# Kernel tuning notes

Measured on AMD Instinct MI355X. Metric: run time of the kernel, lower is better.

Reference implementation:

```python
import jax, jax.numpy as jnp
import numpy as np

B, T, D, H = 4, 2048, 128, 8
HS = D // H          # head_size = 16
E, K = 8, 2          # n_experts, top_experts
FF = 4 * D           # expert hidden = 512
EPS = 1e-5


def setup_inputs() -> dict:
    key = jax.random.key(0)
    ks = jax.random.split(key, 10)
    s = 0.02
    return {
        "x": jax.random.normal(ks[0], (B, T, D), jnp.float32),
        "ln1_g": jnp.ones((D,), jnp.float32),
        "ln1_b": jnp.zeros((D,), jnp.float32),
        "wq": jax.random.normal(ks[1], (H, D, HS), jnp.float32) * s,
        "wk": jax.random.normal(ks[2], (H, D, HS), jnp.float32) * s,
        "wv": jax.random.normal(ks[3], (H, D, HS), jnp.float32) * s,
        "w_proj": jax.random.normal(ks[4], (D, D), jnp.float32) * s,
        "b_proj": jnp.zeros((D,), jnp.float32),
        "ln2_g": jnp.ones((D,), jnp.float32),
        "ln2_b": jnp.zeros((D,), jnp.float32),
        "w_gate": jax.random.normal(ks[5], (D, E), jnp.float32) * s,
        "w1": jax.random.normal(ks[6], (E, D, FF), jnp.float32) * s,
        "b1": jnp.zeros((E, FF), jnp.float32),
        "w2": jax.random.normal(ks[7], (E, FF, D), jnp.float32) * s,
        "b2": jnp.zeros((E, D), jnp.float32),
    }


def _layernorm(x, g, b):
    m = jnp.mean(x, axis=-1, keepdims=True)
    v = jnp.mean(jnp.square(x - m), axis=-1, keepdims=True)
    return (x - m) * jax.lax.rsqrt(v + EPS) * g + b


def reference(x, ln1_g, ln1_b, wq, wk, wv, w_proj, b_proj,
              ln2_g, ln2_b, w_gate, w1, b1, w2, b2):
    Bx, Tx, Dx = x.shape
    # --- attention (pre-LN) ---
    xn = _layernorm(x, ln1_g, ln1_b)
    q = jnp.einsum('btd,hde->bhte', xn, wq)
    k = jnp.einsum('btd,hde->bhte', xn, wk)
    v = jnp.einsum('btd,hde->bhte', xn, wv)
    scale = 1.0 / jnp.sqrt(jnp.asarray(HS, x.dtype))
    scores = jnp.einsum('bhte,bhse->bhts', q, k) * scale  # [B,H,T,T]
    causal = jnp.tril(jnp.ones((Tx, Tx), bool))
    scores = jnp.where(causal, scores, jnp.finfo(x.dtype).min)
    p = jax.nn.softmax(scores, axis=-1)
    attn = jnp.einsum('bhts,bhse->bthe', p, v).reshape(Bx, Tx, Dx)
    x = x + attn @ w_proj + b_proj
    # --- MoE feed-forward (pre-LN) ---
    xn2 = _layernorm(x, ln2_g, ln2_b)
    xf = xn2.reshape(-1, Dx)                 # [N, D], N = B*T
    logits = xf @ w_gate                     # [N, E]
    probs = jax.nn.softmax(logits, axis=-1)
    topv, topi = jax.lax.top_k(probs, K)     # [N, K]
    gate_w = topv / jnp.sum(topv, axis=-1, keepdims=True)
    # expert FFN evaluated densely per expert (grouped-GEMM equivalent)
    h = jax.nn.gelu(jnp.einsum('nd,edh->neh', xf, w1) + b1, approximate=False)
    eo = jnp.einsum('neh,ehd->ned', h, w2) + b2           # [N, E, D]
    sel = jnp.take_along_axis(eo, topi[:, :, None], axis=1)  # [N, K, D]
    ff = jnp.sum(gate_w[:, :, None] * sel, axis=1).reshape(x.shape)
    # Switch-style load-balancing aux loss
    f_e = jnp.sum(jax.nn.one_hot(topi, E, dtype=x.dtype), axis=(0, 1)) / (xf.shape[0] * K)
    p_e = jnp.mean(probs, axis=0)
    aux = E * jnp.sum(f_e * p_e)
    return x + ff, aux
```

## Files before the change

### kernel.cpp

```cpp
#include <hip/hip_runtime.h>
#include <math.h>

#define Bsz 4
#define T 2048
#define D 128
#define H 8
#define HS 16
#define E 8
#define FF 512
#define N (Bsz*T)
#define NQ (Bsz*H*T)
#define EPS 1e-5f
#define SCALE2 0.36067376f
#define SPLITS 8

typedef _Float16 h4 __attribute__((ext_vector_type(4)));
typedef _Float16 h2 __attribute__((ext_vector_type(2)));
typedef float f4 __attribute__((ext_vector_type(4)));
#define MFMA16 __builtin_amdgcn_mfma_f32_16x16x16f16
#define EXP2(x) __builtin_amdgcn_exp2f(x)

__device__ __forceinline__ float wave_sum(float v) {
#pragma unroll
  for (int off = 32; off >= 1; off >>= 1) v += __shfl_xor(v, off);
  return v;
}

__global__ void pack_moe(const float* __restrict__ w1, const float* __restrict__ w2,
                         _Float16* __restrict__ w1pk, _Float16* __restrict__ w2pk) {
  int ft = blockIdx.x, kd = blockIdx.y;
  int e = blockIdx.z >> 1, m = blockIdx.z & 1;
  int l = threadIdx.x, lg = l >> 4, lr = l & 15;
  h4 v;
  if (m == 0) {
    const float* src = w1 + (size_t)e * D * FF;
#pragma unroll
    for (int i = 0; i < 4; ++i)
      v[i] = (_Float16)src[(size_t)(16 * kd + 4 * lg + i) * FF + 16 * ft + lr];
    ((h4*)w1pk)[(((size_t)e * 32 + ft) * 8 + kd) * 64 + l] = v;
  } else {
    const float* src = w2 + (size_t)e * FF * D;
#pragma unroll
    for (int i = 0; i < 4; ++i)
      v[i] = (_Float16)src[(size_t)(16 * ft + 4 * lg + i) * D + 16 * kd + lr];
    ((h4*)w2pk)[(((size_t)e * 32 + ft) * 8 + kd) * 64 + l] = v;
  }
}

__global__ void pack_attn(const float* __restrict__ wq, const float* __restrict__ wk,
                          const float* __restrict__ wv, const float* __restrict__ wp,
                          _Float16* __restrict__ wqh, _Float16* __restrict__ wql,
                          _Float16* __restrict__ wph, _Float16* __restrict__ wpl) {
  int ot = blockIdx.x, kd = blockIdx.y, m = blockIdx.z;
  int l = threadIdx.x, lg = l >> 4, lr = l & 15;
  h4 vh, vl;
  if (m < 3) {
    const float* W = (m == 0 ? wq : (m == 1 ? wk : wv));
    float sc = (m == 0) ? SCALE2 : 1.f;
#pragma unroll
    for (int i = 0; i < 4; ++i) {
      float w = W[((size_t)ot * D + 16 * kd + 4 * lg + i) * HS + lr] * sc;
      _Float16 h = (_Float16)w;
      vh[i] = h;
      vl[i] = (_Float16)(w - (float)h);
    }
    size_t idx = (((size_t)m * 8 + ot) * 8 + kd) * 64 + l;
    ((h4*)wqh)[idx] = vh;
    ((h4*)wql)[idx] = vl;
  } else {
#pragma unroll
    for (int i = 0; i < 4; ++i) {
      float w = wp[(size_t)(16 * kd + 4 * lg + i) * D + 16 * ot + lr];
      _Float16 h = (_Float16)w;
      vh[i] = h;
      vl[i] = (_Float16)(w - (float)h);
    }
    size_t idx = ((size_t)ot * 8 + kd) * 64 + l;
    ((h4*)wph)[idx] = vh;
    ((h4*)wpl)[idx] = vl;
  }
}

__global__ __launch_bounds__(512) void qkv_mfma(
    const float* __restrict__ x, const float* __restrict__ g, const float* __restrict__ bln,
    const _Float16* __restrict__ wh, const _Float16* __restrict__ wl,
    _Float16* __restrict__ qh, _Float16* __restrict__ kh, _Float16* __restrict__ vTh) {
  __shared__ _Float16 xsh[16][136];
  __shared__ _Float16 xsl[16][136];
  int n0 = blockIdx.x * 16;
  int b = n0 >> 11, t0 = n0 & (T - 1);
  int tid = threadIdx.x;
  {
    int i = tid >> 5, c = tid & 31;
    float4 v = *(const float4*)(x + (size_t)(n0 + i) * D + 4 * c);
    float s  = v.x + v.y + v.z + v.w;
    float s2 = v.x*v.x + v.y*v.y + v.z*v.z + v.w*v.w;
#pragma unroll
    for (int off = 16; off >= 1; off >>= 1) { s += __shfl_xor(s, off); s2 += __shfl_xor(s2, off); }
    float m = s * (1.f / D);
    float var = s2 * (1.f / D) - m * m;
    float r = rsqrtf(var + EPS);
    float4 gg = *(const float4*)(g + 4 * c);
    float4 bb = *(const float4*)(bln + 4 * c);
    float o0 = (v.x - m) * r * gg.x + bb.x;
    float o1 = (v.y - m) * r * gg.y + bb.y;
    float o2 = (v.z - m) * r * gg.z + bb.z;
    float o3 = (v.w - m) * r * gg.w + bb.w;
    _Float16 h0 = (_Float16)o0, h1 = (_Float16)o1, h2_ = (_Float16)o2, h3 = (_Float16)o3;
    *(h4*)&xsh[i][4 * c] = (h4){h0, h1, h2_, h3};
    *(h4*)&xsl[i][4 * c] = (h4){(_Float16)(o0 - (float)h0), (_Float16)(o1 - (float)h1),
                                (_Float16)(o2 - (float)h2_), (_Float16)(o3 - (float)h3)};
  }
  __syncthreads();
  int ot = tid >> 6;
  int l = tid & 63, lg = l >> 4, lr = l & 15;
  h4 xfh[8], xfl[8];
#pragma unroll
  for (int kd = 0; kd < 8; ++kd) {
    xfh[kd] = *(const h4*)&xsh[lr][16 * kd + 4 * lg];
    xfl[kd] = *(const h4*)&xsl[lr][16 * kd + 4 * lg];
  }
  const h4* wbh = (const h4*)wh + l;
  const h4* wbl = (const h4*)wl + l;
  f4 aq = {0.f,0.f,0.f,0.f}, ak = aq, av = aq;
#pragma unroll
  for (int kd = 0; kd < 8; ++kd) {
    h4 wqh_ = wbh[((0 * 8 + ot) * 8 + kd) * 64];
    h4 wkh_ = wbh[((1 * 8 + ot) * 8 + kd) * 64];
    h4 wvh_ = wbh[((2 * 8 + ot) * 8 + kd) * 64];
    h4 wql_ = wbl[((0 * 8 + ot) * 8 + kd) * 64];
    h4 wkl_ = wbl[((1 * 8 + ot) * 8 + kd) * 64];
    h4 wvl_ = wbl[((2 * 8 + ot) * 8 + kd) * 64];
    aq = MFMA16(wqh_, xfh[kd], aq, 0, 0, 0);
    ak = MFMA16(wkh_, xfh[kd], ak, 0, 0, 0);
    av = MFMA16(xfh[kd], wvh_, av, 0, 0, 0);
    aq = MFMA16(wql_, xfh[kd], aq, 0, 0, 0);
    ak = MFMA16(wkl_, xfh[kd], ak, 0, 0, 0);
    av = MFMA16(xfl[kd], wvh_, av, 0, 0, 0);
    aq = MFMA16(wqh_, xfl[kd], aq, 0, 0, 0);
    ak = MFMA16(wkh_, xfl[kd], ak, 0, 0, 0);
    av = MFMA16(xfh[kd], wvl_, av, 0, 0, 0);
  }
  h4 q4 = {(_Float16)aq.x, (_Float16)aq.y, (_Float16)aq.z, (_Float16)aq.w};
  h4 k4 = {(_Float16)ak.x, (_Float16)ak.y, (_Float16)ak.z, (_Float16)ak.w};
  size_t qoff = ((size_t)(b * H + ot) * T + t0 + lr) * 16 + 4 * lg;
  *(h4*)(qh + qoff) = q4;
  *(h4*)(kh + qoff) = k4;
  h4 v4 = {(_Float16)av.x, (_Float16)av.y, (_Float16)av.z, (_Float16)av.w};
  *(h4*)(vTh + ((size_t)(b * H + ot) * 16 + lr) * T + t0 + 4 * lg) = v4;
}

__global__ __launch_bounds__(256) void attn_mfma(
    const _Float16* __restrict__ q, const _Float16* __restrict__ k,
    const _Float16* __restrict__ vT, float* __restrict__ part) {
  int bh = blockIdx.y;
  int p = blockIdx.x * 4 + (threadIdx.x >> 6);
  int c = 1;
  while (p >= 2 * c * (c - 1) + 4 * c) ++c;
  int rem = p - 2 * c * (c - 1);
  int qt = (c - 1) * 4 + rem / c;
  int s = rem % c;
  int glo = 4 * s;
  int ghi = min(glo + 4, qt + 1);
  int l = threadIdx.x & 63;
  int lg = l >> 4, lr = l & 15;
  int q0 = qt * 64;
  const h4* qp = (const h4*)(q + ((size_t)bh * T + q0 + lr) * 16 + 4 * lg);
  h4 qf[4];
#pragma unroll
  for (int nt = 0; nt < 4; ++nt) qf[nt] = qp[nt * 64];
  f4 o0 = {0.f,0.f,0.f,0.f}, o1 = o0, o2 = o0, o3 = o0;
  float L0 = 0.f, L1 = 0.f, L2 = 0.f, L3 = 0.f;
  h4 kf[4], vf[4], kf2[4], vf2[4];
#define LOADKV(G, KK, VV) do { \
    int k0g = (G) * 64; \
    const h4* kp = (const h4*)(k + ((size_t)bh * T + k0g + lr) * 16 + 4 * lg); \
    _Pragma("unroll") for (int mt = 0; mt < 4; ++mt) KK[mt] = kp[mt * 64]; \
    const h4* vp = (const h4*)(vT + ((size_t)bh * 16 + lr) * T + k0g + 4 * lg); \
    _Pragma("unroll") for (int mt = 0; mt < 4; ++mt) VV[mt] = vp[mt * 4]; \
  } while (0)
  LOADKV(glo, kf, vf);
  for (int g = glo; g < ghi; ++g) {
    bool more = (g + 1 < ghi);
    if (more) LOADKV(g + 1, kf2, vf2);
    f4 z = {0.f,0.f,0.f,0.f};
    f4 sc[4][4];
#pragma unroll
    for (int mt = 0; mt < 4; ++mt)
#pragma unroll
      for (int nt = 0; nt < 4; ++nt)
        sc[mt][nt] = MFMA16(kf[mt], qf[nt], z, 0, 0, 0);
    if (g == qt) {
#pragma unroll
      for (int mt = 0; mt < 4; ++mt)
#pragma unroll
        for (int nt = 0; nt < 4; ++nt) {
          int kb = 16 * mt + 4 * lg, qb = 16 * nt + lr;
          if (kb + 0 > qb) sc[mt][nt].x = -1e30f;
          if (kb + 1 > qb) sc[mt][nt].y = -1e30f;
          if (kb + 2 > qb) sc[mt][nt].z = -1e30f;
          if (kb + 3 > qb) sc[mt][nt].w = -1e30f;
        }
    }
#define PROC(NT, L, O) do { \
    h4 pf[4]; \
    _Pragma("unroll") for (int mt = 0; mt < 4; ++mt) { \
      f4 a = sc[mt][NT]; h4 pv; float ex; \
      ex = EXP2(a.x); L += ex; pv.x = (_Float16)ex; \
      ex = EXP2(a.y); L += ex; pv.y = (_Float16)ex; \
      ex = EXP2(a.z); L += ex; pv.z = (_Float16)ex; \
      ex = EXP2(a.w); L += ex; pv.w = (_Float16)ex; \
      pf[mt] = pv; } \
    _Pragma("unroll") for (int mt = 0; mt < 4; ++mt) \
      O = MFMA16(vf[mt], pf[mt], O, 0, 0, 0); \
  } while (0)
    PROC(0, L0, o0);
    PROC(1, L1, o1);
    PROC(2, L2, o2);
    PROC(3, L3, o3);
#undef PROC
    if (more) {
#pragma unroll
      for (int mt = 0; mt < 4; ++mt) { kf[mt] = kf2[mt]; vf[mt] = vf2[mt]; }
    }
  }
#undef LOADKV
  L0 += __shfl_xor(L0, 16); L0 += __shfl_xor(L0, 32);
  L1 += __shfl_xor(L1, 16); L1 += __shfl_xor(L1, 32);
  L2 += __shfl_xor(L2, 16); L2 += __shfl_xor(L2, 32);
  L3 += __shfl_xor(L3, 16); L3 += __shfl_xor(L3, 32);
  float* pb = part + (size_t)s * 18 * NQ;
  int nbase = bh * T + q0 + lr;
#define WR(NT, L, O) do { int n = nbase + 16 * NT; \
    pb[(4 * lg + 0) * NQ + n] = O.x; pb[(4 * lg + 1) * NQ + n] = O.y; \
    pb[(4 * lg + 2) * NQ + n] = O.z; pb[(4 * lg + 3) * NQ + n] = O.w; \
    if (lg == 0) pb[16 * NQ + n] = L; \
  } while (0)
  WR(0, L0, o0);
  WR(1, L1, o1);
  WR(2, L2, o2);
  WR(3, L3, o3);
#undef WR
}

__global__ __launch_bounds__(512) void comb_proj(
    const float* __restrict__ part,
    const _Float16* __restrict__ wpph, const _Float16* __restrict__ wppl,
    const float* __restrict__ bp, const float* __restrict__ x,
    const float* __restrict__ ln2g, const float* __restrict__ ln2b,
    float* __restrict__ x1, float* __restrict__ xn2, _Float16* __restrict__ xh) {
  __shared__ float xP[16][132];
  int n0 = blockIdx.x * 16;
  int b = n0 >> 11, t0 = n0 & (T - 1);
  int tid = threadIdx.x;
  int ns = (t0 >> 8) + 1;
  {
    int i = tid & 15, h = (tid >> 4) & 7, r = tid >> 7;
    int n = (b * H + h) * T + t0 + i;
    float a0 = 0.f, a1 = 0.f, a2 = 0.f, a3 = 0.f, L = 0.f;
    for (int s = 0; s < ns; ++s) {
      const float* pb = part + (size_t)s * 18 * NQ;
      L  += pb[16 * NQ + n];
      a0 += pb[(4 * r + 0) * NQ + n];
      a1 += pb[(4 * r + 1) * NQ + n];
      a2 += pb[(4 * r + 2) * NQ + n];
      a3 += pb[(4 * r + 3) * NQ + n];
    }
    float inv = 1.f / L;
    float4 o = {a0 * inv, a1 * inv, a2 * inv, a3 * inv};
    *(float4*)&xP[i][h * 16 + 4 * r] = o;
  }
  __syncthreads();
  int ot = tid >> 6;
  int l = tid & 63, lg = l >> 4, lr = l & 15;
  h4 afh[8], afl[8];
#pragma unroll
  for (int kd = 0; kd < 8; ++kd) {
    float4 v = *(const float4*)&xP[lr][16 * kd + 4 * lg];
    _Float16 h0 = (_Float16)v.x, h1 = (_Float16)v.y, h2_ = (_Float16)v.z, h3 = (_Float16)v.w;
    afh[kd] = (h4){h0, h1, h2_, h3};
    afl[kd] = (h4){(_Float16)(v.x - (float)h0), (_Float16)(v.y - (float)h1),
                   (_Float16)(v.z - (float)h2_), (_Float16)(v.w - (float)h3)};
  }
  const h4* wbh = (const h4*)wpph + l;
  const h4* wbl = (const h4*)wppl + l;
  f4 acc = {0.f,0.f,0.f,0.f};
#pragma unroll
  for (int kd = 0; kd < 8; ++kd) {
    h4 wh_ = wbh[(ot * 8 + kd) * 64];
    h4 wl_ = wbl[(ot * 8 + kd) * 64];
    acc = MFMA16(wh_, afh[kd], acc, 0, 0, 0);
    acc = MFMA16(wl_, afh[kd], acc, 0, 0, 0);
    acc = MFMA16(wh_, afl[kd], acc, 0, 0, 0);
  }
  int o = 16 * ot + 4 * lg;
  float4 xr = *(const float4*)(x + (size_t)(n0 + lr) * D + o);
  float4 bb = *(const float4*)(bp + o);
  float4 ov = {acc.x + xr.x + bb.x, acc.y + xr.y + bb.y,
               acc.z + xr.z + bb.z, acc.w + xr.w + bb.w};
  *(float4*)(x1 + (size_t)(n0 + lr) * D + o) = ov;
  __syncthreads();
  *(float4*)&xP[lr][o] = ov;
  __syncthreads();
  {
    int i = tid >> 5, c = tid & 31;
    float4 v = *(const float4*)&xP[i][4 * c];
    float s  = v.x + v.y + v.z + v.w;
    float s2 = v.x*v.x + v.y*v.y + v.z*v.z + v.w*v.w;
#pragma unroll
    for (int off = 16; off >= 1; off >>= 1) { s += __shfl_xor(s, off); s2 += __shfl_xor(s2, off); }
    float m = s * (1.f / D);
    float var = s2 * (1.f / D) - m * m;
    float r = rsqrtf(var + EPS);
    float4 gg = *(const float4*)(ln2g + 4 * c);
    float4 bv = *(const float4*)(ln2b + 4 * c);
    float4 on = {(v.x - m) * r * gg.x + bv.x, (v.y - m) * r * gg.y + bv.y,
                 (v.z - m) * r * gg.z + bv.z, (v.w - m) * r * gg.w + bv.w};
    *(float4*)(xn2 + (size_t)(n0 + i) * D + 4 * c) = on;
    h4 oh = {(_Float16)on.x, (_Float16)on.y, (_Float16)on.z, (_Float16)on.w};
    *(h4*)(xh + (size_t)(n0 + i) * D + 4 * c) = oh;
  }
}

__global__ void gate_part(const float* __restrict__ xn2, const float* __restrict__ wg,
                          int* __restrict__ wcnt, float* __restrict__ wpsum,
                          int4* __restrict__ tokinfo, float2* __restrict__ gws) {
  int lane = threadIdx.x;
  int blk = blockIdx.x;
  int n = blk * 64 + lane;
  const float4* xr = (const float4*)(xn2 + (size_t)n * D);
  float lg[E];
#pragma unroll
  for (int e = 0; e < E; ++e) lg[e] = 0.f;
  for (int dq = 0; dq < 32; ++dq) {
    float4 xv = xr[dq];
    int d = dq * 4;
#pragma unroll
    for (int e = 0; e < E; ++e)
      lg[e] += xv.x * wg[d*E + e] + xv.y * wg[(d+1)*E + e]
             + xv.z * wg[(d+2)*E + e] + xv.w * wg[(d+3)*E + e];
  }
  float mx = lg[0];
#pragma unroll
  for (int e = 1; e < E; ++e) mx = fmaxf(mx, lg[e]);
  float p[E]; float s = 0.f;
#pragma unroll
  for (int e = 0; e < E; ++e) { p[e] = __expf(lg[e] - mx); s += p[e]; }
  float invs = 1.f / s;
#pragma unroll
  for (int e = 0; e < E; ++e) p[e] *= invs;
#pragma unroll
  for (int e = 0; e < E; ++e) {
    float ve = wave_sum(p[e]);
    if (lane == 0) wpsum[blk * E + e] = ve;
  }
  int i1 = 0; float p1 = p[0];
#pragma unroll
  for (int e = 1; e < E; ++e) if (p[e] > p1) { p1 = p[e]; i1 = e; }
  int i2 = (i1 == 0) ? 1 : 0; float p2 = p[i2];
#pragma unroll
  for (int e = 0; e < E; ++e) if (e != i1 && p[e] > p2) { p2 = p[e]; i2 = e; }
  float gden = 1.f / (p1 + p2);
  unsigned long long lt = (1ULL << lane) - 1ULL;
  int woff0 = 0, woff1 = 0;
  int c0[E], ctot[E];
#pragma unroll
  for (int e = 0; e < E; ++e) {
    unsigned long long m0 = __ballot(i1 == e);
    c0[e] = __popcll(m0);
    if (i1 == e) woff0 = __popcll(m0 & lt);
  }
#pragma unroll
  for (int e = 0; e < E; ++e) {
    unsigned long long m1 = __ballot(i2 == e);
    if (i2 == e) woff1 = c0[e] + __popcll(m1 & lt);
    ctot[e] = c0[e] + __popcll(m1);
  }
  if (lane == 0) {
#pragma unroll
    for (int e = 0; e < E; ++e) wcnt[blk * E + e] = ctot[e];
  }
  tokinfo[n] = make_int4(i1, woff0, i2, woff1);
  gws[n] = make_float2(p1 * gden, p2 * gden);
}

__global__ void gate_scan(const int* __restrict__ wcnt, const float* __restrict__ wpsum,
                          int* __restrict__ wbase, int* __restrict__ ecnt,
                          float* __restrict__ psum) {
  __shared__ int sc[128 * E];
  __shared__ float sp[128 * E];
  int tid = threadIdx.x;
  for (int i = tid; i < 128 * E; i += 64) { sc[i] = wcnt[i]; sp[i] = wpsum[i]; }
  __syncthreads();
  if (tid < E) {
    int run = 0;
    for (int b = 0; b < 128; ++b) { wbase[b * E + tid] = run; run += sc[b * E + tid]; }
    ecnt[tid] = run;
  } else if (tid >= 16 && tid < 16 + E) {
    int e = tid - 16;
    float sum = 0.f;
    for (int b = 0; b < 128; ++b) sum += sp[b * E + e];
    psum[e] = sum;
  }
}

__global__ void gate_scatter(const int4* __restrict__ tokinfo, const float2* __restrict__ gws,
                             const int* __restrict__ wbase,
                             int* __restrict__ ltok, int* __restrict__ sidx,
                             float* __restrict__ gwn) {
  int lane = threadIdx.x;
  int blk = blockIdx.x;
  int n = blk * 64 + lane;
  int4 ti = tokinfo[n];
  float2 g = gws[n];
  int pos0 = wbase[blk * E + ti.x] + ti.y;
  int pos1 = wbase[blk * E + ti.z] + ti.w;
  ltok[ti.x * N + pos0] = n;
  ltok[ti.z * N + pos1] = n;
  sidx[2 * n]     = ti.x * N + pos0;
  sidx[2 * n + 1] = ti.z * N + pos1;
  gwn[2 * n]     = g.x;
  gwn[2 * n + 1] = g.y;
}

__global__ __launch_bounds__(256) void moe_mfma(
    const _Float16* __restrict__ xh, const _Float16* __restrict__ w1pk,
    const float* __restrict__ b1, const _Float16* __restrict__ w2pk,
    const float* __restrict__ b2, const int* __restrict__ ecnt,
    const int* __restrict__ ltok, float* __restrict__ eo) {
  int e = blockIdx.y;
  int cnt = ecnt[e];
  int t0 = blockIdx.x * 16;
  if (t0 >= cnt) return;
  __shared__ int toks[16];
  __shared__ f4 red[3][8][64];
  int tid = threadIdx.x;
  if (tid < 16)
    toks[tid] = (t0 + tid < cnt) ? ltok[e * N + t0 + tid] : -1;
  __syncthreads();
  int fh = tid >> 6;
  int l = tid & 63;
  int lg = l >> 4, lr = l & 15;
  int tok = toks[lr];
  const h4* xp = (const h4*)(xh + (size_t)(tok < 0 ? 0 : tok) * D + 4 * lg);
  h4 xf[8];
#pragma unroll
  for (int kd = 0; kd < 8; ++kd) xf[kd] = xp[kd * 4];
  f4 oacc[8];
#pragma unroll
  for (int dt = 0; dt < 8; ++dt) oacc[dt] = (f4){0.f,0.f,0.f,0.f};
  const float* b1e = b1 + e * FF;
  const h4* w1b = (const h4*)w1pk + ((size_t)e * 32 + 8 * fh) * 8 * 64 + l;
  const h4* w2b = (const h4*)w2pk + ((size_t)e * 32 + 8 * fh) * 8 * 64 + l;
#pragma unroll 2
  for (int ftl = 0; ftl < 8; ++ftl) {
    f4 ha = {0.f,0.f,0.f,0.f};
#pragma unroll
    for (int kd = 0; kd < 8; ++kd)
      ha = MFMA16(w1b[(ftl * 8 + kd) * 64], xf[kd], ha, 0, 0, 0);
    int ft = 8 * fh + ftl;
    float4 bb = *(const float4*)&b1e[16 * ft + 4 * lg];
    h4 pf;
    {
      float z;
      z = ha.x + bb.x; pf.x = (_Float16)(0.5f * z * (1.f + erff(z * 0.70710678f)));
      z = ha.y + bb.y; pf.y = (_Float16)(0.5f * z * (1.f + erff(z * 0.70710678f)));
      z = ha.z + bb.z; pf.z = (_Float16)(0.5f * z * (1.f + erff(z * 0.70710678f)));
      z = ha.w + bb.w; pf.w = (_Float16)(0.5f * z * (1.f + erff(z * 0.70710678f)));
    }
#pragma unroll
    for (int dt = 0; dt < 8; ++dt)
      oacc[dt] = MFMA16(w2b[(ftl * 8 + dt) * 64], pf, oacc[dt], 0, 0, 0);
  }
  if (fh >= 1) {
#pragma unroll
    for (int dt = 0; dt < 8; ++dt) red[fh - 1][dt][l] = oacc[dt];
  }
  __syncthreads();
  if (fh == 0 && tok >= 0) {
    const float* b2e = b2 + e * D;
    float* eop = eo + ((size_t)(e * N + t0 + lr)) * 128;
#pragma unroll
    for (int dt = 0; dt < 8; ++dt) {
      f4 r0 = red[0][dt][l], r1 = red[1][dt][l], r2 = red[2][dt][l];
      float4 bb = *(const float4*)&b2e[16 * dt + 4 * lg];
      float4 o4 = {oacc[dt].x + r0.x + r1.x + r2.x + bb.x,
                   oacc[dt].y + r0.y + r1.y + r2.y + bb.y,
                   oacc[dt].z + r0.z + r1.z + r2.z + bb.z,
                   oacc[dt].w + r0.w + r1.w + r2.w + bb.w};
      *(float4*)(eop + 16 * dt + 4 * lg) = o4;
    }
  }
}

__global__ void finalize_kernel(const float* __restrict__ x1, const float* __restrict__ eo,
                                const int* __restrict__ sidx, const float* __restrict__ gwn,
                                const float* __restrict__ psum, const int* __restrict__ ecnt,
                                float* __restrict__ out) {
  int idx = blockIdx.x * 256 + threadIdx.x;
  int n = idx >> 5, d4 = idx & 31;
  int i0 = sidx[2*n], i1 = sidx[2*n+1];
  float g0 = gwn[2*n], g1 = gwn[2*n+1];
  float4 a = ((const float4*)x1)[idx];
  float4 u = ((const float4*)eo)[(size_t)i0 * 32 + d4];
  float4 w = ((const float4*)eo)[(size_t)i1 * 32 + d4];
  float4 o = {a.x + g0*u.x + g1*w.x, a.y + g0*u.y + g1*w.y,
              a.z + g0*u.z + g1*w.z, a.w + g0*u.w + g1*w.w};
  ((float4*)out)[idx] = o;
  if (idx == 0) {
    float aux = 0.f;
    for (int e = 0; e < E; ++e)
      aux += ((float)ecnt[e] * (1.f / 16384.f)) * (psum[e] * (1.f / 8192.f));
    out[N * D] = 8.f * aux;
  }
}

extern "C" void kernel_launch(void* const* d_in, const int* in_sizes, int n_in,
                              void* d_out, int out_size, void* d_ws, size_t ws_size,
                              hipStream_t stream) {
  const float* x    = (const float*)d_in[0];
  const float* ln1g = (const float*)d_in[1];
  const float* ln1b = (const float*)d_in[2];
  const float* wq   = (const float*)d_in[3];
  const float* wk   = (const float*)d_in[4];
  const float* wv   = (const float*)d_in[5];
  const float* wp   = (const float*)d_in[6];
  const float* bp   = (const float*)d_in[7];
  const float* ln2g = (const float*)d_in[8];
  const float* ln2b = (const float*)d_in[9];
  const float* wg   = (const float*)d_in[10];
  const float* w1   = (const float*)d_in[11];
  const float* b1   = (const float*)d_in[12];
  const float* w2   = (const float*)d_in[13];
  const float* b2   = (const float*)d_in[14];
  float* out = (float*)d_out;
  float* ws = (float*)d_ws;
  const size_t M = 1u << 20;
  float* Bq = ws + 1 * M;
  _Float16* qh  = (_Float16*)(ws + 2 * M);
  _Float16* xh  = (_Float16*)(ws + 2 * M);
  _Float16* kh  = (_Float16*)(ws + 2 * M + M / 2);
  _Float16* vTh = (_Float16*)(ws + 3 * M);
  float* part = ws + 3 * M + M / 2;
  float* eo   = part;
  float* xn2  = ws + 13 * M + M / 2;
  _Float16* w1pk = (_Float16*)(ws + 14 * M + M / 2);
  _Float16* w2pk = (_Float16*)(ws + 14 * M + 3 * (M / 4));
  size_t G0 = 15 * M;
  int*    ltok   = (int*)(ws + G0);
  int*    sidx   = (int*)(ws + G0 + 65536);
  float*  gwn    = ws + G0 + 81920;
  float*  psum   = ws + G0 + 98304;
  int*    ecnt   = (int*)(ws + G0 + 98312);
  int*    wcnt   = (int*)(ws + G0 + 98320);
  float*  wpsum  = ws + G0 + 99344;
  int*    wbase  = (int*)(ws + G0 + 100368);
  int4*   tokinfo= (int4*)(ws + G0 + 101392);
  float2* gws    = (float2*)(ws + G0 + 134160);
  _Float16* wqkvh = (_Float16*)(ws + G0 + 150544);
  _Float16* wqkvl = (_Float16*)(ws + G0 + 175120);
  _Float16* wpph  = (_Float16*)(ws + G0 + 199696);
  _Float16* wppl  = (_Float16*)(ws + G0 + 207888);

  pack_moe<<<dim3(32, 8, 2 * E), 64, 0, stream>>>(w1, w2, w1pk, w2pk);
  pack_attn<<<dim3(8, 8, 4), 64, 0, stream>>>(wq, wk, wv, wp, wqkvh, wqkvl, wpph, wppl);
  qkv_mfma<<<N / 16, 512, 0, stream>>>(x, ln1g, ln1b, wqkvh, wqkvl, qh, kh, vTh);
  attn_mfma<<<dim3(36, Bsz * H), 256, 0, stream>>>(qh, kh, vTh, part);
  comb_proj<<<N / 16, 512, 0, stream>>>(part, wpph, wppl, bp, x, ln2g, ln2b, Bq, xn2, xh);
  gate_part<<<N / 64, 64, 0, stream>>>(xn2, wg, wcnt, wpsum, tokinfo, gws);
  gate_scan<<<1, 64, 0, stream>>>(wcnt, wpsum, wbase, ecnt, psum);
  gate_scatter<<<N / 64, 64, 0, stream>>>(tokinfo, gws, wbase, ltok, sidx, gwn);
  moe_mfma<<<dim3(N / 16, E), 256, 0, stream>>>(xh, w1pk, b1, w2pk, b2, ecnt, ltok, eo);
  finalize_kernel<<<(N * D / 4) / 256, 256, 0, stream>>>(Bq, eo, sidx, gwn, psum, ecnt, out);
}
```

Baseline: 112.3 us.

## Fuse gating into comb_proj and merge scan with scatter kernel

Gate logits, softmax, top-2 selection and per-block counting now run inside comb_proj on the LN2 output held in shared memory, so the fp32 xn2 buffer is neither written nor re-read. The single-block scan and the scatter kernel are merged into one kernel in which every block redundantly reloads all 512 per-block counts and computes the prefix sums itself. This cuts the launch count by two and removes a serial single-block step. The cost is that only 16 threads do the gating work in comb_proj, and each scatter block repeats the scan.

After: 115.7 us. +3.0%, slower.

```diff
diff --git a/kernel.cpp b/kernel.cpp
--- a/kernel.cpp
+++ b/kernel.cpp
@@ -19,12 +19,6 @@
 typedef float f4 __attribute__((ext_vector_type(4)));
 #define MFMA16 __builtin_amdgcn_mfma_f32_16x16x16f16
 #define EXP2(x) __builtin_amdgcn_exp2f(x)
-
-__device__ __forceinline__ float wave_sum(float v) {
-#pragma unroll
-  for (int off = 32; off >= 1; off >>= 1) v += __shfl_xor(v, off);
-  return v;
-}
 
 __global__ void pack_moe(const float* __restrict__ w1, const float* __restrict__ w2,
                          _Float16* __restrict__ w1pk, _Float16* __restrict__ w2pk) {
@@ -248,10 +242,14 @@
     const _Float16* __restrict__ wpph, const _Float16* __restrict__ wppl,
     const float* __restrict__ bp, const float* __restrict__ x,
     const float* __restrict__ ln2g, const float* __restrict__ ln2b,
-    float* __restrict__ x1, float* __restrict__ xn2, _Float16* __restrict__ xh) {
+    const float* __restrict__ wg,
+    float* __restrict__ x1, _Float16* __restrict__ xh,
+    int* __restrict__ wcnt, float* __restrict__ wpsum,
+    int4* __restrict__ tokinfo, float2* __restrict__ gws) {
   __shared__ float xP[16][132];
   int n0 = blockIdx.x * 16;
   int b = n0 >> 11, t0 = n0 & (T - 1);
+  int blk = blockIdx.x;
   int tid = threadIdx.x;
   int ns = (t0 >> 8) + 1;
   {
@@ -316,105 +314,113 @@
     float4 bv = *(const float4*)(ln2b + 4 * c);
     float4 on = {(v.x - m) * r * gg.x + bv.x, (v.y - m) * r * gg.y + bv.y,
                  (v.z - m) * r * gg.z + bv.z, (v.w - m) * r * gg.w + bv.w};
-    *(float4*)(xn2 + (size_t)(n0 + i) * D + 4 * c) = on;
     h4 oh = {(_Float16)on.x, (_Float16)on.y, (_Float16)on.z, (_Float16)on.w};
     *(h4*)(xh + (size_t)(n0 + i) * D + 4 * c) = oh;
-  }
-}
-
-__global__ void gate_part(const float* __restrict__ xn2, const float* __restrict__ wg,
-                          int* __restrict__ wcnt, float* __restrict__ wpsum,
-                          int4* __restrict__ tokinfo, float2* __restrict__ gws) {
-  int lane = threadIdx.x;
-  int blk = blockIdx.x;
-  int n = blk * 64 + lane;
-  const float4* xr = (const float4*)(xn2 + (size_t)n * D);
-  float lg[E];
-#pragma unroll
-  for (int e = 0; e < E; ++e) lg[e] = 0.f;
-  for (int dq = 0; dq < 32; ++dq) {
-    float4 xv = xr[dq];
-    int d = dq * 4;
-#pragma unroll
-    for (int e = 0; e < E; ++e)
-      lg[e] += xv.x * wg[d*E + e] + xv.y * wg[(d+1)*E + e]
-             + xv.z * wg[(d+2)*E + e] + xv.w * wg[(d+3)*E + e];
-  }
-  float mx = lg[0];
-#pragma unroll
-  for (int e = 1; e < E; ++e) mx = fmaxf(mx, lg[e]);
-  float p[E]; float s = 0.f;
-#pragma unroll
-  for (int e = 0; e < E; ++e) { p[e] = __expf(lg[e] - mx); s += p[e]; }
-  float invs = 1.f / s;
-#pragma unroll
-  for (int e = 0; e < E; ++e) p[e] *= invs;
-#pragma unroll
-  for (int e = 0; e < E; ++e) {
-    float ve = wave_sum(p[e]);
-    if (lane == 0) wpsum[blk * E + e] = ve;
-  }
-  int i1 = 0; float p1 = p[0];
-#pragma unroll
-  for (int e = 1; e < E; ++e) if (p[e] > p1) { p1 = p[e]; i1 = e; }
-  int i2 = (i1 == 0) ? 1 : 0; float p2 = p[i2];
-#pragma unroll
-  for (int e = 0; e < E; ++e) if (e != i1 && p[e] > p2) { p2 = p[e]; i2 = e; }
-  float gden = 1.f / (p1 + p2);
-  unsigned long long lt = (1ULL << lane) - 1ULL;
-  int woff0 = 0, woff1 = 0;
-  int c0[E], ctot[E];
-#pragma unroll
-  for (int e = 0; e < E; ++e) {
-    unsigned long long m0 = __ballot(i1 == e);
-    c0[e] = __popcll(m0);
-    if (i1 == e) woff0 = __popcll(m0 & lt);
-  }
-#pragma unroll
-  for (int e = 0; e < E; ++e) {
-    unsigned long long m1 = __ballot(i2 == e);
-    if (i2 == e) woff1 = c0[e] + __popcll(m1 & lt);
-    ctot[e] = c0[e] + __popcll(m1);
-  }
-  if (lane == 0) {
-#pragma unroll
-    for (int e = 0; e < E; ++e) wcnt[blk * E + e] = ctot[e];
-  }
-  tokinfo[n] = make_int4(i1, woff0, i2, woff1);
-  gws[n] = make_float2(p1 * gden, p2 * gden);
-}
-
-__global__ void gate_scan(const int* __restrict__ wcnt, const float* __restrict__ wpsum,
-                          int* __restrict__ wbase, int* __restrict__ ecnt,
-                          float* __restrict__ psum) {
-  __shared__ int sc[128 * E];
-  __shared__ float sp[128 * E];
-  int tid = threadIdx.x;
-  for (int i = tid; i < 128 * E; i += 64) { sc[i] = wcnt[i]; sp[i] = wpsum[i]; }
-  __syncthreads();
-  if (tid < E) {
+    *(float4*)&xP[i][4 * c] = on;
+  }
+  __syncthreads();
+  if (tid < 16) {
+    int n = n0 + tid;
+    float lgt[E];
+#pragma unroll
+    for (int e = 0; e < E; ++e) lgt[e] = 0.f;
+    for (int dq = 0; dq < 32; ++dq) {
+      float4 xv = *(const float4*)&xP[tid][4 * dq];
+      int d = dq * 4;
+#pragma unroll
+      for (int e = 0; e < E; ++e)
+        lgt[e] += xv.x * wg[d*E + e] + xv.y * wg[(d+1)*E + e]
+                + xv.z * wg[(d+2)*E + e] + xv.w * wg[(d+3)*E + e];
+    }
+    float mx = lgt[0];
+#pragma unroll
+    for (int e = 1; e < E; ++e) mx = fmaxf(mx, lgt[e]);
+    float p[E]; float s = 0.f;
+#pragma unroll
+    for (int e = 0; e < E; ++e) { p[e] = __expf(lgt[e] - mx); s += p[e]; }
+    float invs = 1.f / s;
+#pragma unroll
+    for (int e = 0; e < E; ++e) p[e] *= invs;
+#pragma unroll
+    for (int e = 0; e < E; ++e) {
+      float ve = p[e];
+      ve += __shfl_xor(ve, 8); ve += __shfl_xor(ve, 4);
+      ve += __shfl_xor(ve, 2); ve += __shfl_xor(ve, 1);
+      if (tid == 0) wpsum[blk * E + e] = ve;
+    }
+    int i1 = 0; float p1 = p[0];
+#pragma unroll
+    for (int e = 1; e < E; ++e) if (p[e] > p1) { p1 = p[e]; i1 = e; }
+    int i2 = (i1 == 0) ? 1 : 0; float p2 = p[i2];
+#pragma unroll
+    for (int e = 0; e < E; ++e) if (e != i1 && p[e] > p2) { p2 = p[e]; i2 = e; }
+    float gden = 1.f / (p1 + p2);
+    unsigned long long lt = (1ULL << tid) - 1ULL;
+    int woff0 = 0, woff1 = 0;
+    int c0[E], ctot[E];
+#pragma unroll
+    for (int e = 0; e < E; ++e) {
+      unsigned long long m0 = __ballot(i1 == e);
+      c0[e] = __popcll(m0);
+      if (i1 == e) woff0 = __popcll(m0 & lt);
+    }
+#pragma unroll
+    for (int e = 0; e < E; ++e) {
+      unsigned long long m1 = __ballot(i2 == e);
+      if (i2 == e) woff1 = c0[e] + __popcll(m1 & lt);
+      ctot[e] = c0[e] + __popcll(m1);
+    }
+    if (tid == 0) {
+#pragma unroll
+      for (int e = 0; e < E; ++e) wcnt[blk * E + e] = ctot[e];
+    }
+    tokinfo[n] = make_int4(i1, woff0, i2, woff1);
+    gws[n] = make_float2(p1 * gden, p2 * gden);
+  }
+}
+
+__global__ __launch_bounds__(64) void gate_scat(
+    const int* __restrict__ wcnt, const float* __restrict__ wpsum,
+    const int4* __restrict__ tokinfo, const float2* __restrict__ gws,
+    int* __restrict__ ltok, int* __restrict__ sidx, float* __restrict__ gwn,
+    int* __restrict__ ecnt, float* __restrict__ psum) {
+  __shared__ int pre[512 * E];
+  __shared__ int segsum[8][E];
+  int tid = threadIdx.x, blk = blockIdx.x;
+  for (int i = tid; i < 512 * E; i += 64) pre[i] = wcnt[i];
+  __syncthreads();
+  {
+    int e = tid & 7, seg = tid >> 3;
+    int s = 0;
+    for (int b = seg * 64; b < seg * 64 + 64; ++b) s += pre[b * E + e];
+    segsum[seg][e] = s;
+  }
+  __syncthreads();
+  if (tid < 8) {
     int run = 0;
-    for (int b = 0; b < 128; ++b) { wbase[b * E + tid] = run; run += sc[b * E + tid]; }
-    ecnt[tid] = run;
-  } else if (tid >= 16 && tid < 16 + E) {
+    for (int g = 0; g < 8; ++g) { int c = segsum[g][tid]; segsum[g][tid] = run; run += c; }
+    if (blk == 0) ecnt[tid] = run;
+  } else if (blk == 0 && tid >= 16 && tid < 24) {
     int e = tid - 16;
-    float sum = 0.f;
-    for (int b = 0; b < 128; ++b) sum += sp[b * E + e];
-    psum[e] = sum;
-  }
-}
-
-__global__ void gate_scatter(const int4* __restrict__ tokinfo, const float2* __restrict__ gws,
-                             const int* __restrict__ wbase,
-                             int* __restrict__ ltok, int* __restrict__ sidx,
-                             float* __restrict__ gwn) {
-  int lane = threadIdx.x;
-  int blk = blockIdx.x;
-  int n = blk * 64 + lane;
+    float s = 0.f;
+    for (int b = 0; b < 512; ++b) s += wpsum[b * E + e];
+    psum[e] = s;
+  }
+  __syncthreads();
+  {
+    int e = tid & 7, seg = tid >> 3;
+    int run = segsum[seg][e];
+    for (int b = seg * 64; b < seg * 64 + 64; ++b) {
+      int c = pre[b * E + e]; pre[b * E + e] = run; run += c;
+    }
+  }
+  __syncthreads();
+  int n = blk * 64 + tid;
   int4 ti = tokinfo[n];
   float2 g = gws[n];
-  int pos0 = wbase[blk * E + ti.x] + ti.y;
-  int pos1 = wbase[blk * E + ti.z] + ti.w;
+  int sb = n >> 4;
+  int pos0 = pre[sb * E + ti.x] + ti.y;
+  int pos1 = pre[sb * E + ti.z] + ti.w;
   ltok[ti.x * N + pos0] = n;
   ltok[ti.z * N + pos1] = n;
   sidx[2 * n]     = ti.x * N + pos0;
@@ -543,7 +549,6 @@
   _Float16* vTh = (_Float16*)(ws + 3 * M);
   float* part = ws + 3 * M + M / 2;
   float* eo   = part;
-  float* xn2  = ws + 13 * M + M / 2;
   _Float16* w1pk = (_Float16*)(ws + 14 * M + M / 2);
   _Float16* w2pk = (_Float16*)(ws + 14 * M + 3 * (M / 4));
   size_t G0 = 15 * M;
@@ -553,23 +558,21 @@
   float*  psum   = ws + G0 + 98304;
   int*    ecnt   = (int*)(ws + G0 + 98312);
   int*    wcnt   = (int*)(ws + G0 + 98320);
-  float*  wpsum  = ws + G0 + 99344;
-  int*    wbase  = (int*)(ws + G0 + 100368);
-  int4*   tokinfo= (int4*)(ws + G0 + 101392);
-  float2* gws    = (float2*)(ws + G0 + 134160);
-  _Float16* wqkvh = (_Float16*)(ws + G0 + 150544);
-  _Float16* wqkvl = (_Float16*)(ws + G0 + 175120);
-  _Float16* wpph  = (_Float16*)(ws + G0 + 199696);
-  _Float16* wppl  = (_Float16*)(ws + G0 + 207888);
+  float*  wpsum  = ws + G0 + 102416;
+  int4*   tokinfo= (int4*)(ws + G0 + 106512);
+  float2* gws    = (float2*)(ws + G0 + 139280);
+  _Float16* wqkvh = (_Float16*)(ws + G0 + 155664);
+  _Float16* wqkvl = (_Float16*)(ws + G0 + 180240);
+  _Float16* wpph  = (_Float16*)(ws + G0 + 204816);
+  _Float16* wppl  = (_Float16*)(ws + G0 + 213008);
 
   pack_moe<<<dim3(32, 8, 2 * E), 64, 0, stream>>>(w1, w2, w1pk, w2pk);
   pack_attn<<<dim3(8, 8, 4), 64, 0, stream>>>(wq, wk, wv, wp, wqkvh, wqkvl, wpph, wppl);
   qkv_mfma<<<N / 16, 512, 0, stream>>>(x, ln1g, ln1b, wqkvh, wqkvl, qh, kh, vTh);
   attn_mfma<<<dim3(36, Bsz * H), 256, 0, stream>>>(qh, kh, vTh, part);
-  comb_proj<<<N / 16, 512, 0, stream>>>(part, wpph, wppl, bp, x, ln2g, ln2b, Bq, xn2, xh);
-  gate_part<<<N / 64, 64, 0, stream>>>(xn2, wg, wcnt, wpsum, tokinfo, gws);
-  gate_scan<<<1, 64, 0, stream>>>(wcnt, wpsum, wbase, ecnt, psum);
-  gate_scatter<<<N / 64, 64, 0, stream>>>(tokinfo, gws, wbase, ltok, sidx, gwn);
+  comb_proj<<<N / 16, 512, 0, stream>>>(part, wpph, wppl, bp, x, ln2g, ln2b, wg,
+                                        Bq, xh, wcnt, wpsum, tokinfo, gws);
+  gate_scat<<<N / 64, 64, 0, stream>>>(wcnt, wpsum, tokinfo, gws, ltok, sidx, gwn, ecnt, psum);
   moe_mfma<<<dim3(N / 16, E), 256, 0, stream>>>(xh, w1pk, b1, w2pk, b2, ecnt, ltok, eo);
   finalize_kernel<<<(N * D / 4) / 256, 256, 0, stream>>>(Bq, eo, sidx, gwn, psum, ecnt, out);
 }
```
